# Kernel tuning notes

Hardware: AMD Instinct MI355X
Metric: run time of the kernel (lower is better)

The kernel has to match this reference:

```python
import jax, jax.numpy as jnp
import numpy as np

H = 384          # hidden_dim == filter_size == n_chans
N_BINS = 256
PRED_GRAD = 0.1
LN_EPS = 1e-5


def _conv1d_same(x_bct, w_oik, b):
    k = w_oik.shape[-1]
    p = (k - 1) // 2
    y = jax.lax.conv_general_dilated(
        x_bct, w_oik, window_strides=(1,), padding=[(p, p)],
        dimension_numbers=("NCT", "OIT", "NCT"))
    return y + b[None, :, None]


def _ln_last(x, g, b):  # LayerNorm over last dim
    m = jnp.mean(x, axis=-1, keepdims=True)
    v = jnp.var(x, axis=-1, keepdims=True)
    return (x - m) * jax.lax.rsqrt(v + LN_EPS) * g + b


def _ln_chan(x_bct, g, b):  # LayerNorm over channel dim (dim=1)
    m = jnp.mean(x_bct, axis=1, keepdims=True)
    v = jnp.var(x_bct, axis=1, keepdims=True)
    return (x_bct - m) * jax.lax.rsqrt(v + LN_EPS) * g[None, :, None] + b[None, :, None]


def _sin_pos(x0, dim):
    # fairseq SinusoidalPositionalEmbedding, padding_idx=0, applied to xs[...,0]
    mask = (x0 != 0).astype(jnp.int32)
    pos = jnp.cumsum(mask, axis=1) * mask                        # [B,T]
    half = dim // 2
    inv = jnp.exp(jnp.arange(half, dtype=jnp.float32) * (-(np.log(10000.0) / (half - 1))))
    ang = pos[..., None].astype(jnp.float32) * inv               # [B,T,half]
    pe = jnp.concatenate([jnp.sin(ang), jnp.cos(ang)], axis=-1)  # [B,T,dim]
    return jnp.where(pos[..., None] == 0, 0.0, pe)


def _duration_predictor(x, src_mask, w1, b1, g1, be1, w2, b2, g2, be2, lw, lb):
    h = _conv1d_same(jnp.swapaxes(x, 1, 2), w1, b1)
    h = _ln_last(jax.nn.relu(jnp.swapaxes(h, 1, 2)), g1, be1)
    h = _conv1d_same(jnp.swapaxes(h, 1, 2), w2, b2)
    h = _ln_last(jax.nn.relu(jnp.swapaxes(h, 1, 2)), g2, be2)
    out = (h @ lw + lb)[..., 0]                                  # [B,T]
    return jnp.where(src_mask, 0.0, out)


def _variance_predictor(x, cw, cb, g, b, lw, lb, alpha):
    pos = alpha * _sin_pos(x[..., 0], x.shape[-1])
    h = jnp.swapaxes(x + pos, 1, 2)                              # [B,C,T]
    for i in range(cw.shape[0]):
        h = _ln_chan(jax.nn.relu(_conv1d_same(h, cw[i], cb[i])), g[i], b[i])
    return jnp.swapaxes(h, 1, 2) @ lw + lb                       # [B,T,odim]


def _length_regulate(x, dur_int, max_len):
    B, T, _ = x.shape
    cum = jnp.cumsum(dur_int, axis=1)                            # [B,T]
    frames = jnp.arange(max_len)
    idx = jax.vmap(lambda c: jnp.searchsorted(c, frames, side="right"))(cum)
    idx = jnp.clip(idx, 0, T - 1)                                # [B,max_len]
    out = jnp.take_along_axis(x, idx[..., None], axis=1)         # [B,max_len,H]
    total = cum[:, -1]
    valid = frames[None, :] < total[:, None]
    out = jnp.where(valid[..., None], out, 0.0)
    mel_len = jnp.minimum(total, max_len)
    return out, mel_len


def setup_inputs() -> dict:
    key = jax.random.key(0)
    ks = iter(jax.random.split(key, 40))
    B, T = 32, 1024
    rnd = lambda s: 0.02 * jax.random.normal(next(ks), s, dtype=jnp.float32)
    inp = {
        "x": jax.random.normal(next(ks), (B, T, H), dtype=jnp.float32),
        "src_lens": jax.random.randint(next(ks), (B,), 0, T),
        "src_mask": jnp.zeros((B, T), dtype=bool),
        "max_len": 4096,
        # duration predictor (kernel=3)
        "dp_w1": rnd((H, H, 3)), "dp_b1": jnp.zeros((H,)),
        "dp_ln1_g": jnp.ones((H,)), "dp_ln1_b": jnp.zeros((H,)),
        "dp_w2": rnd((H, H, 3)), "dp_b2": jnp.zeros((H,)),
        "dp_ln2_g": jnp.ones((H,)), "dp_ln2_b": jnp.zeros((H,)),
        "dp_lw": rnd((H, 1)), "dp_lb": jnp.full((1,), 1.5),  # bias -> avg dur ~3.5
        # pitch predictor: 5 layers, kernel=5, odim=1 (use_uv=False)
        "pp_cw": rnd((5, H, H, 5)), "pp_cb": jnp.zeros((5, H)),
        "pp_g": jnp.ones((5, H)), "pp_b": jnp.zeros((5, H)),
        "pp_lw": rnd((H, 1)), "pp_lb": jnp.zeros((1,)), "pp_alpha": jnp.ones((1,)),
        # energy predictor: 2 layers, kernel=5, odim=1
        "ep_cw": rnd((2, H, H, 5)), "ep_cb": jnp.zeros((2, H)),
        "ep_g": jnp.ones((2, H)), "ep_b": jnp.zeros((2, H)),
        "ep_lw": rnd((H, 1)), "ep_lb": jnp.zeros((1,)), "ep_alpha": jnp.ones((1,)),
        # bins (requires_grad=False buffers) + embedding tables
        "pitch_bins": jnp.linspace(-4.0, 4.0, N_BINS - 1),
        "energy_bins": jnp.linspace(-4.0, 4.0, N_BINS - 1),
        "pitch_table": rnd((N_BINS, H)),
        "energy_table": rnd((N_BINS, H)),
    }
    return inp


def reference(x, src_lens, src_mask, max_len,
              dp_w1, dp_b1, dp_ln1_g, dp_ln1_b, dp_w2, dp_b2, dp_ln2_g, dp_ln2_b, dp_lw, dp_lb,
              pp_cw, pp_cb, pp_g, pp_b, pp_lw, pp_lb, pp_alpha,
              ep_cw, ep_cb, ep_g, ep_b, ep_lw, ep_lb, ep_alpha,
              pitch_bins, energy_bins, pitch_table, energy_table):
    # duration (inference path: no targets, controls = 1.0)
    log_d = _duration_predictor(x, src_mask, dp_w1, dp_b1, dp_ln1_g, dp_ln1_b,
                                dp_w2, dp_b2, dp_ln2_g, dp_ln2_b, dp_lw, dp_lb)
    dur = jnp.clip(jnp.round(jnp.exp(log_d) - 1.0), 0.0, None)
    dur_int = dur.astype(jnp.int32)

    # straight-through-style grad scaling on predictor inputs
    xg = jax.lax.stop_gradient(x) + PRED_GRAD * (x - jax.lax.stop_gradient(x))

    # phoneme-level pitch (use_uv=False -> squeeze, bucketize)
    pitch_pred = _variance_predictor(xg, pp_cw, pp_cb, pp_g, pp_b, pp_lw, pp_lb, pp_alpha)[..., 0]
    pitch_idx = jnp.searchsorted(pitch_bins, pitch_pred, side="left")  # torch.bucketize(right=False)
    pitch_emb = pitch_table[pitch_idx]

    # phoneme-level energy
    energy_pred = _variance_predictor(xg, ep_cw, ep_cb, ep_g, ep_b, ep_lw, ep_lb, ep_alpha)[..., 0]
    energy_idx = jnp.searchsorted(energy_bins, energy_pred, side="left")
    energy_emb = energy_table[energy_idx]

    x_adapt = x + pitch_emb + energy_emb
    out, mel_len = _length_regulate(x_adapt, dur_int, int(max_len))
    return out, log_d, dur, pitch_pred, energy_pred, mel_len
```

## Files before the change

kernel.cpp:

```cpp
#include <hip/hip_runtime.h>
#include <cstdint>

#define HH 384
#define NBINS 256

typedef __attribute__((ext_vector_type(8))) short short8v;
typedef __attribute__((ext_vector_type(16))) float f32x16;
typedef __attribute__((ext_vector_type(4))) unsigned short ushort4v;

__device__ inline float4 ld4(const float* p){ return *(const float4*)p; }

__device__ inline unsigned short bf16_rne(float f){
  unsigned u = __float_as_uint(f);
  unsigned r = u + 0x7FFFu + ((u >> 16) & 1u);
  return (unsigned short)(r >> 16);
}
__device__ inline float bf16_to_f(unsigned short h){
  return __uint_as_float(((unsigned)h) << 16);
}

__global__ __launch_bounds__(1024) void pos_kernel(const float* __restrict__ x,
    int* __restrict__ pos, int T)
{
  __shared__ int s[1024];
  int b = blockIdx.x, tid = threadIdx.x;
  int m = 0;
  if (tid < T) m = (x[((size_t)b*T + tid)*HH] != 0.f) ? 1 : 0;
  s[tid] = m;
  __syncthreads();
  for (int off = 1; off < 1024; off <<= 1){
    int add = (tid >= off) ? s[tid-off] : 0;
    __syncthreads();
    s[tid] += add;
    __syncthreads();
  }
  if (tid < T) pos[(size_t)b*T + tid] = s[tid] * m;
}

__global__ __launch_bounds__(HH) void add_pe_kernel(const float* __restrict__ x,
    const int* __restrict__ pos, const float* __restrict__ alpha,
    float* __restrict__ out)
{
  int row = blockIdx.x; int i = threadIdx.x;
  int p = pos[row];
  float pe = 0.f;
  if (p != 0){
    int j = (i < HH/2) ? i : i - HH/2;
    float inv = expf((float)j * -0.04822167734018944f);
    float ang = (float)p * inv;
    pe = (i < HH/2) ? sinf(ang) : cosf(ang);
  }
  out[(size_t)row*HH + i] = x[(size_t)row*HH + i] + alpha[0]*pe;
}

template<int K>
__global__ __launch_bounds__(256) void wtrans_kernel(const float* __restrict__ w,
    unsigned short* __restrict__ whi, unsigned short* __restrict__ wlo)
{
  int gid = blockIdx.x*256 + threadIdx.x;
  if (gid >= 384*384) return;
  int o = gid / 384, i = gid - (gid/384)*384;
  int c = i >> 4, half = (i >> 3) & 1, jj = i & 7;
  #pragma unroll
  for (int k = 0; k < K; ++k){
    float v = w[((size_t)o*384 + i)*K + k];
    unsigned short hi = bf16_rne(v);
    unsigned short lo = bf16_rne(v - bf16_to_f(hi));
    int s = k*24 + c;
    size_t dst = ((size_t)(s*2 + half)*384 + o)*8 + jj;
    whi[dst] = hi; wlo[dst] = lo;
  }
}

template<int K>
__global__ __launch_bounds__(256) void conv_mfma_kernel(
    const float* __restrict__ in, const unsigned short* __restrict__ whi,
    const unsigned short* __restrict__ wlo, const float* __restrict__ bias,
    const float* __restrict__ g, const float* __restrict__ be,
    float* __restrict__ out, int T)
{
  constexpr int M  = 32;
  constexpr int P  = (K-1)/2;
  constexpr int RT = M + K - 1;
  constexpr int NS = 24*K;
  constexpr int LDP = 392;
  __shared__ unsigned short xs_hi[(RT+1)*LDP];
  __shared__ unsigned short xs_lo[(RT+1)*LDP];
  __shared__ float ps[4][M], pq[4][M];

  int ntile = T / M;
  int b  = blockIdx.x / ntile;
  int t0 = (blockIdx.x % ntile) * M;
  int tid = threadIdx.x;
  const float* inb = in + (size_t)b*T*HH;

  {
    constexpr int TOT4 = RT*384/4;
    for (int e4 = tid; e4 < TOT4; e4 += 256){
      int r = e4 / 96, c4 = (e4 - r*96)*4;
      int t = t0 + r - P;
      float4 v = (t >= 0 && t < T) ? ld4(&inb[(size_t)t*HH + c4])
                                   : make_float4(0.f,0.f,0.f,0.f);
      float va[4] = {v.x, v.y, v.z, v.w};
      ushort4v h, l;
      #pragma unroll
      for (int q = 0; q < 4; ++q){
        unsigned short hq = bf16_rne(va[q]);
        h[q] = hq;
        l[q] = bf16_rne(va[q] - bf16_to_f(hq));
      }
      *(ushort4v*)&xs_hi[r*LDP + c4] = h;
      *(ushort4v*)&xs_lo[r*LDP + c4] = l;
    }
  }
  __syncthreads();

  int wv = tid >> 6, ln = tid & 63;
  int l31 = ln & 31, hl = ln >> 5;
  int o0 = wv * 96;

  const unsigned short* bhp = whi + ((size_t)hl*384 + o0 + l31)*8;
  const unsigned short* blp = wlo + ((size_t)hl*384 + o0 + l31)*8;
  int ab = l31*LDP + hl*8;

  f32x16 acc[3];
  #pragma unroll
  for (int nt = 0; nt < 3; ++nt){
    float bv = bias[o0 + nt*32 + l31];
    #pragma unroll
    for (int r = 0; r < 16; ++r) acc[nt][r] = bv;
  }

  short8v B0h[3], B0l[3], B1h[3], B1l[3];
  short8v A0h, A0l, A1h, A1l;

  #pragma unroll
  for (int nt = 0; nt < 3; ++nt){
    B0h[nt] = *(const short8v*)(bhp + nt*256);
    B0l[nt] = *(const short8v*)(blp + nt*256);
  }
  A0h = *(const short8v*)&xs_hi[ab];
  A0l = *(const short8v*)&xs_lo[ab];

  int aoffN = ab, ccN = 0;

#define CONV_STEP(CAh, CAl, CBh, CBl, NAh, NAl, NBh, NBl)                     \
  do {                                                                        \
    bhp += 6144; blp += 6144;                                                 \
    aoffN += 16; if (++ccN == 24){ ccN = 0; aoffN += LDP - 384; }             \
    _Pragma("unroll")                                                         \
    for (int nt = 0; nt < 3; ++nt){                                           \
      (NBh)[nt] = *(const short8v*)(bhp + nt*256);                            \
      (NBl)[nt] = *(const short8v*)(blp + nt*256);                            \
    }                                                                         \
    (NAh) = *(const short8v*)&xs_hi[aoffN];                                   \
    (NAl) = *(const short8v*)&xs_lo[aoffN];                                   \
    __builtin_amdgcn_sched_barrier(0);                                        \
    __builtin_amdgcn_s_setprio(1);                                            \
    _Pragma("unroll")                                                         \
    for (int nt = 0; nt < 3; ++nt)                                            \
      acc[nt] = __builtin_amdgcn_mfma_f32_32x32x16_bf16((CAh), (CBh)[nt], acc[nt], 0,0,0); \
    _Pragma("unroll")                                                         \
    for (int nt = 0; nt < 3; ++nt)                                            \
      acc[nt] = __builtin_amdgcn_mfma_f32_32x32x16_bf16((CAh), (CBl)[nt], acc[nt], 0,0,0); \
    _Pragma("unroll")                                                         \
    for (int nt = 0; nt < 3; ++nt)                                            \
      acc[nt] = __builtin_amdgcn_mfma_f32_32x32x16_bf16((CAl), (CBh)[nt], acc[nt], 0,0,0); \
    __builtin_amdgcn_s_setprio(0);                                            \
  } while(0)

  for (int s = 0; s < NS; s += 2){
    CONV_STEP(A0h, A0l, B0h, B0l, A1h, A1l, B1h, B1l);
    CONV_STEP(A1h, A1l, B1h, B1l, A0h, A0l, B0h, B0l);
  }
#undef CONV_STEP

  float gv[3], bev[3];
  #pragma unroll
  for (int nt = 0; nt < 3; ++nt){
    gv[nt]  = g[o0 + nt*32 + l31];
    bev[nt] = be[o0 + nt*32 + l31];
  }

  #pragma unroll
  for (int r = 0; r < 16; ++r){
    float s1 = 0.f, s2 = 0.f;
    #pragma unroll
    for (int nt = 0; nt < 3; ++nt){
      float v = fmaxf(acc[nt][r], 0.f);
      acc[nt][r] = v;
      s1 += v; s2 += v*v;
    }
    s1 += __shfl_xor(s1, 1);  s2 += __shfl_xor(s2, 1);
    s1 += __shfl_xor(s1, 2);  s2 += __shfl_xor(s2, 2);
    s1 += __shfl_xor(s1, 4);  s2 += __shfl_xor(s2, 4);
    s1 += __shfl_xor(s1, 8);  s2 += __shfl_xor(s2, 8);
    s1 += __shfl_xor(s1, 16); s2 += __shfl_xor(s2, 16);
    if (l31 == 0){
      int t = (r&3) + 8*(r>>2) + 4*hl;
      ps[wv][t] = s1; pq[wv][t] = s2;
    }
  }
  __syncthreads();

  #pragma unroll
  for (int r = 0; r < 16; ++r){
    int t = (r&3) + 8*(r>>2) + 4*hl;
    float s1 = ps[0][t] + ps[1][t] + ps[2][t] + ps[3][t];
    float s2 = pq[0][t] + pq[1][t] + pq[2][t] + pq[3][t];
    float mn  = s1 * (1.f/HH);
    float var = fmaxf(s2 * (1.f/HH) - mn*mn, 0.f);
    float rr  = rsqrtf(var + 1e-5f);
    float* orow = out + ((size_t)b*T + t0 + t)*HH;
    #pragma unroll
    for (int nt = 0; nt < 3; ++nt)
      orow[o0 + nt*32 + l31] = (acc[nt][r] - mn)*rr*gv[nt] + bev[nt];
  }
}

__global__ __launch_bounds__(256) void proj_var_kernel(const float* __restrict__ h,
    const float* __restrict__ lw, const float* __restrict__ lb,
    const float* __restrict__ bins, float* __restrict__ pred,
    int* __restrict__ idx, int nrows)
{
  int lane = threadIdx.x & 63, wid = threadIdx.x >> 6;
  int wave = blockIdx.x*4 + wid, nw = gridDim.x*4;
  float lwr[6];
  #pragma unroll
  for (int j = 0; j < 6; ++j) lwr[j] = lw[lane + 64*j];
  float lbv = lb[0];
  for (int row = wave; row < nrows; row += nw){
    const float* hr = h + (size_t)row*HH;
    float s = 0.f;
    #pragma unroll
    for (int j = 0; j < 6; ++j) s = fmaf(hr[lane + 64*j], lwr[j], s);
    #pragma unroll
    for (int off = 32; off; off >>= 1) s += __shfl_xor(s, off);
    if (lane == 0){
      float v = s + lbv;
      pred[row] = v;
      int lo = 0, hi = NBINS - 1;
      while (lo < hi){ int mid = (lo + hi) >> 1; if (bins[mid] < v) lo = mid + 1; else hi = mid; }
      idx[row] = lo;
    }
  }
}

__global__ __launch_bounds__(256) void proj_dur_kernel(const float* __restrict__ h,
    const float* __restrict__ lw, const float* __restrict__ lb,
    const unsigned char* __restrict__ mask, float* __restrict__ logd,
    float* __restrict__ durf, int* __restrict__ duri, int nrows)
{
  int lane = threadIdx.x & 63, wid = threadIdx.x >> 6;
  int wave = blockIdx.x*4 + wid, nw = gridDim.x*4;
  float lwr[6];
  #pragma unroll
  for (int j = 0; j < 6; ++j) lwr[j] = lw[lane + 64*j];
  float lbv = lb[0];
  for (int row = wave; row < nrows; row += nw){
    const float* hr = h + (size_t)row*HH;
    float s = 0.f;
    #pragma unroll
    for (int j = 0; j < 6; ++j) s = fmaf(hr[lane + 64*j], lwr[j], s);
    #pragma unroll
    for (int off = 32; off; off >>= 1) s += __shfl_xor(s, off);
    if (lane == 0){
      float v = s + lbv;
      if (mask[row]) v = 0.f;
      logd[row] = v;
      float d = fmaxf(rintf(expf(v) - 1.f), 0.f);
      durf[row] = d;
      duri[row] = (int)d;
    }
  }
}

__global__ __launch_bounds__(1024) void cumsum_kernel(const int* __restrict__ duri,
    int* __restrict__ cum, float* __restrict__ mel, int T, int ML)
{
  __shared__ int s[1024];
  int b = blockIdx.x, tid = threadIdx.x;
  s[tid] = (tid < T) ? duri[(size_t)b*T + tid] : 0;
  __syncthreads();
  for (int off = 1; off < 1024; off <<= 1){
    int add = (tid >= off) ? s[tid-off] : 0;
    __syncthreads();
    s[tid] += add;
    __syncthreads();
  }
  if (tid < T) cum[(size_t)b*T + tid] = s[tid];
  if (tid == T-1) mel[b] = (float)min(s[tid], ML);
}

__global__ __launch_bounds__(256) void xadapt_kernel(const float* __restrict__ x,
    const int* __restrict__ ip, const int* __restrict__ ie,
    const float* __restrict__ pt, const float* __restrict__ et,
    float* __restrict__ xa, int nrows)
{
  int gid = blockIdx.x*256 + threadIdx.x;
  int n4 = nrows * (HH/4);
  if (gid >= n4) return;
  int row = gid / (HH/4);
  int c = gid - row*(HH/4);
  float4 xv = ((const float4*)x)[gid];
  const float4* pr = (const float4*)(pt + (size_t)ip[row]*HH);
  const float4* er = (const float4*)(et + (size_t)ie[row]*HH);
  float4 pv = pr[c], ev = er[c];
  ((float4*)xa)[gid] = make_float4(xv.x+pv.x+ev.x, xv.y+pv.y+ev.y,
                                   xv.z+pv.z+ev.z, xv.w+pv.w+ev.w);
}

__global__ __launch_bounds__(256) void lr_kernel(const float* __restrict__ xa,
    const int* __restrict__ cum, float* __restrict__ out, int T, int ML)
{
  constexpr int FR = 32;
  __shared__ int scum[1024];
  __shared__ int sidx[FR];
  __shared__ int svalid[FR];
  int b  = blockIdx.y;
  int f0 = blockIdx.x * FR;
  for (int i = threadIdx.x; i < T; i += 256) scum[i] = cum[(size_t)b*T + i];
  __syncthreads();
  int total = scum[T-1];
  if (threadIdx.x < FR){
    int f = f0 + threadIdx.x;
    int lo = 0, hi = T;
    while (lo < hi){ int mid = (lo + hi) >> 1; if (scum[mid] <= f) lo = mid + 1; else hi = mid; }
    sidx[threadIdx.x] = min(lo, T-1);
    svalid[threadIdx.x] = (f < total) ? 1 : 0;
  }
  __syncthreads();
  #pragma unroll
  for (int it = 0; it < FR*(HH/4)/256; ++it){
    int item = it*256 + threadIdx.x;
    int fl = item / (HH/4);
    int c  = item - fl*(HH/4);
    int f  = f0 + fl;
    if (f >= ML) continue;
    float4 v = make_float4(0.f,0.f,0.f,0.f);
    if (svalid[fl]) v = ((const float4*)(xa + ((size_t)b*T + sidx[fl])*HH))[c];
    ((float4*)(out + ((size_t)b*ML + f)*HH))[c] = v;
  }
}

extern "C" void kernel_launch(void* const* d_in, const int* in_sizes, int n_in,
                              void* d_out, int out_size, void* d_ws, size_t ws_size,
                              hipStream_t stream)
{
  const float* x        = (const float*)d_in[0];
  const unsigned char* src_mask = (const unsigned char*)d_in[2];
  const float* dp_w1 = (const float*)d_in[4];
  const float* dp_b1 = (const float*)d_in[5];
  const float* dp_g1 = (const float*)d_in[6];
  const float* dp_be1= (const float*)d_in[7];
  const float* dp_w2 = (const float*)d_in[8];
  const float* dp_b2 = (const float*)d_in[9];
  const float* dp_g2 = (const float*)d_in[10];
  const float* dp_be2= (const float*)d_in[11];
  const float* dp_lw = (const float*)d_in[12];
  const float* dp_lb = (const float*)d_in[13];
  const float* pp_cw = (const float*)d_in[14];
  const float* pp_cb = (const float*)d_in[15];
  const float* pp_g  = (const float*)d_in[16];
  const float* pp_b  = (const float*)d_in[17];
  const float* pp_lw = (const float*)d_in[18];
  const float* pp_lb = (const float*)d_in[19];
  const float* pp_alpha = (const float*)d_in[20];
  const float* ep_cw = (const float*)d_in[21];
  const float* ep_cb = (const float*)d_in[22];
  const float* ep_g  = (const float*)d_in[23];
  const float* ep_b  = (const float*)d_in[24];
  const float* ep_lw = (const float*)d_in[25];
  const float* ep_lb = (const float*)d_in[26];
  const float* ep_alpha = (const float*)d_in[27];
  const float* pbins = (const float*)d_in[28];
  const float* ebins = (const float*)d_in[29];
  const float* ptab  = (const float*)d_in[30];
  const float* etab  = (const float*)d_in[31];

  int B = in_sizes[1];
  int T = in_sizes[0] / (B*HH);
  int ML = (int)(((long long)out_size - B - 4LL*B*T) / ((long long)B*HH));
  size_t rows = (size_t)B*T;

  float* bufA = (float*)d_ws;
  float* bufB = bufA + rows*HH;
  int* pos    = (int*)(bufB + rows*HH);
  int* idx_p  = pos + rows;
  int* idx_e  = idx_p + rows;
  int* dur_i  = idx_e + rows;
  int* cum    = dur_i + rows;

  float* out0    = (float*)d_out;
  float* logd    = out0 + (size_t)B*ML*HH;
  float* durf    = logd + rows;
  float* pitchp  = durf + rows;
  float* energyp = pitchp + rows;
  float* mel     = energyp + rows;

  unsigned short* wsc = (unsigned short*)d_out;
  const size_t K5S = (size_t)120*6144;
  const size_t K3S = (size_t)72*6144;
  size_t woff = 0;
  unsigned short *pph[5], *ppl[5], *eph[2], *epl[2], *dph[2], *dpl[2];
  for (int l = 0; l < 5; ++l){ pph[l] = wsc + woff; woff += K5S; ppl[l] = wsc + woff; woff += K5S; }
  for (int l = 0; l < 2; ++l){ eph[l] = wsc + woff; woff += K5S; epl[l] = wsc + woff; woff += K5S; }
  for (int l = 0; l < 2; ++l){ dph[l] = wsc + woff; woff += K3S; dpl[l] = wsc + woff; woff += K3S; }

  int wt_grid = (384*384 + 255)/256;
  for (int l = 0; l < 5; ++l)
    wtrans_kernel<5><<<wt_grid, 256, 0, stream>>>(pp_cw + (size_t)l*HH*HH*5, pph[l], ppl[l]);
  for (int l = 0; l < 2; ++l)
    wtrans_kernel<5><<<wt_grid, 256, 0, stream>>>(ep_cw + (size_t)l*HH*HH*5, eph[l], epl[l]);
  wtrans_kernel<3><<<wt_grid, 256, 0, stream>>>(dp_w1, dph[0], dpl[0]);
  wtrans_kernel<3><<<wt_grid, 256, 0, stream>>>(dp_w2, dph[1], dpl[1]);

  int conv_grid = B * (T / 32);

  pos_kernel<<<B, 1024, 0, stream>>>(x, pos, T);

  add_pe_kernel<<<(int)rows, HH, 0, stream>>>(x, pos, pp_alpha, bufA);
  {
    float* src = bufA; float* dst = bufB;
    for (int l = 0; l < 5; ++l){
      conv_mfma_kernel<5><<<conv_grid, 256, 0, stream>>>(src, pph[l], ppl[l],
          pp_cb + (size_t)l*HH, pp_g + (size_t)l*HH, pp_b + (size_t)l*HH, dst, T);
      float* t2 = dst; dst = src; src = t2;
    }
    proj_var_kernel<<<256, 256, 0, stream>>>(src, pp_lw, pp_lb, pbins,
                                             pitchp, idx_p, (int)rows);
  }

  add_pe_kernel<<<(int)rows, HH, 0, stream>>>(x, pos, ep_alpha, bufA);
  {
    float* src = bufA; float* dst = bufB;
    for (int l = 0; l < 2; ++l){
      conv_mfma_kernel<5><<<conv_grid, 256, 0, stream>>>(src, eph[l], epl[l],
          ep_cb + (size_t)l*HH, ep_g + (size_t)l*HH, ep_b + (size_t)l*HH, dst, T);
      float* t2 = dst; dst = src; src = t2;
    }
    proj_var_kernel<<<256, 256, 0, stream>>>(src, ep_lw, ep_lb, ebins,
                                             energyp, idx_e, (int)rows);
  }

  conv_mfma_kernel<3><<<conv_grid, 256, 0, stream>>>(x, dph[0], dpl[0],
      dp_b1, dp_g1, dp_be1, bufB, T);
  conv_mfma_kernel<3><<<conv_grid, 256, 0, stream>>>(bufB, dph[1], dpl[1],
      dp_b2, dp_g2, dp_be2, bufA, T);
  proj_dur_kernel<<<256, 256, 0, stream>>>(bufA, dp_lw, dp_lb, src_mask,
                                           logd, durf, dur_i, (int)rows);

  cumsum_kernel<<<B, 1024, 0, stream>>>(dur_i, cum, mel, T, ML);

  xadapt_kernel<<<(int)((rows*(HH/4) + 255)/256), 256, 0, stream>>>(
      x, idx_p, idx_e, ptab, etab, bufB, (int)rows);

  lr_kernel<<<dim3(ML/32, B), 256, 0, stream>>>(bufB, cum, out0, T, ML);
}
```

Baseline: 1.579 ms.

## Double conv time tile to 64 rows with 512 threads and deeper prefetch

The conv kernel now processes 64 time rows per block using 8 waves: two row groups share each weight column slice, so every weight fragment loaded from global memory serves twice as many outputs. The software pipeline now prefetches two steps ahead with triple-buffered registers. Weight transform launches are merged into one launch per predictor, and each layer's weight buffer is padded by two extra slices so the deeper prefetch can read past the end safely. The costs are higher register pressure, fewer blocks for small T, and a requirement that T be a multiple of 64.

```diff
diff --git a/kernel.cpp b/kernel.cpp
--- a/kernel.cpp
+++ b/kernel.cpp
@@ -55,48 +55,55 @@
 
 template<int K>
 __global__ __launch_bounds__(256) void wtrans_kernel(const float* __restrict__ w,
-    unsigned short* __restrict__ whi, unsigned short* __restrict__ wlo)
-{
+    unsigned short* __restrict__ dst, int nlayers)
+{
+  constexpr int SPL = (24*K + 2) * 6144;
+  const int per = 384*384;
   int gid = blockIdx.x*256 + threadIdx.x;
-  if (gid >= 384*384) return;
-  int o = gid / 384, i = gid - (gid/384)*384;
+  if (gid >= nlayers*per) return;
+  int l = gid / per, rem = gid - l*per;
+  int o = rem / 384, i = rem - (rem/384)*384;
+  unsigned short* whi = dst + (size_t)l*2*SPL;
+  unsigned short* wlo = whi + SPL;
+  const float* wl = w + (size_t)l*384*384*K;
   int c = i >> 4, half = (i >> 3) & 1, jj = i & 7;
   #pragma unroll
   for (int k = 0; k < K; ++k){
-    float v = w[((size_t)o*384 + i)*K + k];
+    float v = wl[((size_t)o*384 + i)*K + k];
     unsigned short hi = bf16_rne(v);
     unsigned short lo = bf16_rne(v - bf16_to_f(hi));
     int s = k*24 + c;
-    size_t dst = ((size_t)(s*2 + half)*384 + o)*8 + jj;
-    whi[dst] = hi; wlo[dst] = lo;
+    size_t d = ((size_t)(s*2 + half)*384 + o)*8 + jj;
+    whi[d] = hi; wlo[d] = lo;
   }
 }
 
 template<int K>
-__global__ __launch_bounds__(256) void conv_mfma_kernel(
+__global__ __launch_bounds__(512) void conv_mfma_kernel(
     const float* __restrict__ in, const unsigned short* __restrict__ whi,
     const unsigned short* __restrict__ wlo, const float* __restrict__ bias,
     const float* __restrict__ g, const float* __restrict__ be,
     float* __restrict__ out, int T)
 {
-  constexpr int M  = 32;
+  constexpr int MT = 64;
   constexpr int P  = (K-1)/2;
-  constexpr int RT = M + K - 1;
+  constexpr int RT = MT + K - 1;
+  constexpr int RA = RT + 2;
   constexpr int NS = 24*K;
   constexpr int LDP = 392;
-  __shared__ unsigned short xs_hi[(RT+1)*LDP];
-  __shared__ unsigned short xs_lo[(RT+1)*LDP];
-  __shared__ float ps[4][M], pq[4][M];
-
-  int ntile = T / M;
+  __shared__ unsigned short xs_hi[RA*LDP];
+  __shared__ unsigned short xs_lo[RA*LDP];
+  __shared__ float ps[8][32], pq[8][32];
+
+  int ntile = T / MT;
   int b  = blockIdx.x / ntile;
-  int t0 = (blockIdx.x % ntile) * M;
+  int t0 = (blockIdx.x % ntile) * MT;
   int tid = threadIdx.x;
   const float* inb = in + (size_t)b*T*HH;
 
   {
-    constexpr int TOT4 = RT*384/4;
-    for (int e4 = tid; e4 < TOT4; e4 += 256){
+    constexpr int TOT4 = RT*96;
+    for (int e4 = tid; e4 < TOT4; e4 += 512){
       int r = e4 / 96, c4 = (e4 - r*96)*4;
       int t = t0 + r - P;
       float4 v = (t >= 0 && t < T) ? ld4(&inb[(size_t)t*HH + c4])
@@ -117,11 +124,13 @@
 
   int wv = tid >> 6, ln = tid & 63;
   int l31 = ln & 31, hl = ln >> 5;
-  int o0 = wv * 96;
+  int nw = wv & 3, rg = wv >> 2;
+  int o0 = nw * 96;
 
   const unsigned short* bhp = whi + ((size_t)hl*384 + o0 + l31)*8;
   const unsigned short* blp = wlo + ((size_t)hl*384 + o0 + l31)*8;
-  int ab = l31*LDP + hl*8;
+  int aoff = (rg*32 + l31)*LDP + hl*8;
+  int cc = 0;
 
   f32x16 acc[3];
   #pragma unroll
@@ -131,49 +140,59 @@
     for (int r = 0; r < 16; ++r) acc[nt][r] = bv;
   }
 
-  short8v B0h[3], B0l[3], B1h[3], B1l[3];
-  short8v A0h, A0l, A1h, A1l;
+  short8v B0h[3], B0l[3], B1h[3], B1l[3], B2h[3], B2l[3];
+  short8v A0h, A0l, A1h, A1l, A2h, A2l;
+
+#define ADV do{ bhp += 6144; blp += 6144; aoff += 16;                        \
+                if (++cc == 24){ cc = 0; aoff += LDP - 384; } }while(0)
 
   #pragma unroll
   for (int nt = 0; nt < 3; ++nt){
     B0h[nt] = *(const short8v*)(bhp + nt*256);
     B0l[nt] = *(const short8v*)(blp + nt*256);
   }
-  A0h = *(const short8v*)&xs_hi[ab];
-  A0l = *(const short8v*)&xs_lo[ab];
-
-  int aoffN = ab, ccN = 0;
-
-#define CONV_STEP(CAh, CAl, CBh, CBl, NAh, NAl, NBh, NBl)                     \
-  do {                                                                        \
-    bhp += 6144; blp += 6144;                                                 \
-    aoffN += 16; if (++ccN == 24){ ccN = 0; aoffN += LDP - 384; }             \
-    _Pragma("unroll")                                                         \
-    for (int nt = 0; nt < 3; ++nt){                                           \
-      (NBh)[nt] = *(const short8v*)(bhp + nt*256);                            \
-      (NBl)[nt] = *(const short8v*)(blp + nt*256);                            \
-    }                                                                         \
-    (NAh) = *(const short8v*)&xs_hi[aoffN];                                   \
-    (NAl) = *(const short8v*)&xs_lo[aoffN];                                   \
-    __builtin_amdgcn_sched_barrier(0);                                        \
-    __builtin_amdgcn_s_setprio(1);                                            \
-    _Pragma("unroll")                                                         \
-    for (int nt = 0; nt < 3; ++nt)                                            \
-      acc[nt] = __builtin_amdgcn_mfma_f32_32x32x16_bf16((CAh), (CBh)[nt], acc[nt], 0,0,0); \
-    _Pragma("unroll")                                                         \
-    for (int nt = 0; nt < 3; ++nt)                                            \
-      acc[nt] = __builtin_amdgcn_mfma_f32_32x32x16_bf16((CAh), (CBl)[nt], acc[nt], 0,0,0); \
-    _Pragma("unroll")                                                         \
-    for (int nt = 0; nt < 3; ++nt)                                            \
-      acc[nt] = __builtin_amdgcn_mfma_f32_32x32x16_bf16((CAl), (CBh)[nt], acc[nt], 0,0,0); \
-    __builtin_amdgcn_s_setprio(0);                                            \
+  A0h = *(const short8v*)&xs_hi[aoff];
+  A0l = *(const short8v*)&xs_lo[aoff];
+  ADV;
+  #pragma unroll
+  for (int nt = 0; nt < 3; ++nt){
+    B1h[nt] = *(const short8v*)(bhp + nt*256);
+    B1l[nt] = *(const short8v*)(blp + nt*256);
+  }
+  A1h = *(const short8v*)&xs_hi[aoff];
+  A1l = *(const short8v*)&xs_lo[aoff];
+  ADV;
+
+#define PHASE(NBh,NBl,NAh,NAl,CBh,CBl,CAh,CAl) do{                           \
+    _Pragma("unroll")                                                        \
+    for (int nt = 0; nt < 3; ++nt){                                          \
+      NBh[nt] = *(const short8v*)(bhp + nt*256);                             \
+      NBl[nt] = *(const short8v*)(blp + nt*256);                             \
+    }                                                                        \
+    NAh = *(const short8v*)&xs_hi[aoff];                                     \
+    NAl = *(const short8v*)&xs_lo[aoff];                                     \
+    ADV;                                                                     \
+    __builtin_amdgcn_sched_barrier(0);                                       \
+    __builtin_amdgcn_s_setprio(1);                                           \
+    _Pragma("unroll")                                                        \
+    for (int nt = 0; nt < 3; ++nt)                                           \
+      acc[nt] = __builtin_amdgcn_mfma_f32_32x32x16_bf16(CAh, CBh[nt], acc[nt], 0,0,0); \
+    _Pragma("unroll")                                                        \
+    for (int nt = 0; nt < 3; ++nt)                                           \
+      acc[nt] = __builtin_amdgcn_mfma_f32_32x32x16_bf16(CAh, CBl[nt], acc[nt], 0,0,0); \
+    _Pragma("unroll")                                                        \
+    for (int nt = 0; nt < 3; ++nt)                                           \
+      acc[nt] = __builtin_amdgcn_mfma_f32_32x32x16_bf16(CAl, CBh[nt], acc[nt], 0,0,0); \
+    __builtin_amdgcn_s_setprio(0);                                           \
   } while(0)
 
-  for (int s = 0; s < NS; s += 2){
-    CONV_STEP(A0h, A0l, B0h, B0l, A1h, A1l, B1h, B1l);
-    CONV_STEP(A1h, A1l, B1h, B1l, A0h, A0l, B0h, B0l);
-  }
-#undef CONV_STEP
+  for (int s = 0; s < NS; s += 3){
+    PHASE(B2h,B2l,A2h,A2l, B0h,B0l,A0h,A0l);
+    PHASE(B0h,B0l,A0h,A0l, B1h,B1l,A1h,A1l);
+    PHASE(B1h,B1l,A1h,A1l, B2h,B2l,A2h,A2l);
+  }
+#undef PHASE
+#undef ADV
 
   float gv[3], bev[3];
   #pragma unroll
@@ -206,12 +225,12 @@
   #pragma unroll
   for (int r = 0; r < 16; ++r){
     int t = (r&3) + 8*(r>>2) + 4*hl;
-    float s1 = ps[0][t] + ps[1][t] + ps[2][t] + ps[3][t];
-    float s2 = pq[0][t] + pq[1][t] + pq[2][t] + pq[3][t];
+    float s1 = ps[rg*4+0][t] + ps[rg*4+1][t] + ps[rg*4+2][t] + ps[rg*4+3][t];
+    float s2 = pq[rg*4+0][t] + pq[rg*4+1][t] + pq[rg*4+2][t] + pq[rg*4+3][t];
     float mn  = s1 * (1.f/HH);
     float var = fmaxf(s2 * (1.f/HH) - mn*mn, 0.f);
     float rr  = rsqrtf(var + 1e-5f);
-    float* orow = out + ((size_t)b*T + t0 + t)*HH;
+    float* orow = out + ((size_t)b*T + t0 + rg*32 + t)*HH;
     #pragma unroll
     for (int nt = 0; nt < 3; ++nt)
       orow[o0 + nt*32 + l31] = (acc[nt][r] - mn)*rr*gv[nt] + bev[nt];
@@ -398,24 +417,21 @@
   float* energyp = pitchp + rows;
   float* mel     = energyp + rows;
 
-  unsigned short* wsc = (unsigned short*)d_out;
-  const size_t K5S = (size_t)120*6144;
-  const size_t K3S = (size_t)72*6144;
-  size_t woff = 0;
-  unsigned short *pph[5], *ppl[5], *eph[2], *epl[2], *dph[2], *dpl[2];
-  for (int l = 0; l < 5; ++l){ pph[l] = wsc + woff; woff += K5S; ppl[l] = wsc + woff; woff += K5S; }
-  for (int l = 0; l < 2; ++l){ eph[l] = wsc + woff; woff += K5S; epl[l] = wsc + woff; woff += K5S; }
-  for (int l = 0; l < 2; ++l){ dph[l] = wsc + woff; woff += K3S; dpl[l] = wsc + woff; woff += K3S; }
-
-  int wt_grid = (384*384 + 255)/256;
-  for (int l = 0; l < 5; ++l)
-    wtrans_kernel<5><<<wt_grid, 256, 0, stream>>>(pp_cw + (size_t)l*HH*HH*5, pph[l], ppl[l]);
-  for (int l = 0; l < 2; ++l)
-    wtrans_kernel<5><<<wt_grid, 256, 0, stream>>>(ep_cw + (size_t)l*HH*HH*5, eph[l], epl[l]);
-  wtrans_kernel<3><<<wt_grid, 256, 0, stream>>>(dp_w1, dph[0], dpl[0]);
-  wtrans_kernel<3><<<wt_grid, 256, 0, stream>>>(dp_w2, dph[1], dpl[1]);
-
-  int conv_grid = B * (T / 32);
+  const size_t SPL5 = (size_t)(24*5 + 2)*6144;
+  const size_t SPL3 = (size_t)(24*3 + 2)*6144;
+  unsigned short* wsc    = (unsigned short*)d_out;
+  unsigned short* pitchW = wsc;
+  unsigned short* enerW  = pitchW + 5*2*SPL5;
+  unsigned short* durW1  = enerW  + 2*2*SPL5;
+  unsigned short* durW2  = durW1  + 2*SPL3;
+
+  const int per = 384*384;
+  wtrans_kernel<5><<<(5*per + 255)/256, 256, 0, stream>>>(pp_cw, pitchW, 5);
+  wtrans_kernel<5><<<(2*per + 255)/256, 256, 0, stream>>>(ep_cw, enerW, 2);
+  wtrans_kernel<3><<<(per + 255)/256, 256, 0, stream>>>(dp_w1, durW1, 1);
+  wtrans_kernel<3><<<(per + 255)/256, 256, 0, stream>>>(dp_w2, durW2, 1);
+
+  int conv_grid = B * (T / 64);
 
   pos_kernel<<<B, 1024, 0, stream>>>(x, pos, T);
 
@@ -423,7 +439,8 @@
   {
     float* src = bufA; float* dst = bufB;
     for (int l = 0; l < 5; ++l){
-      conv_mfma_kernel<5><<<conv_grid, 256, 0, stream>>>(src, pph[l], ppl[l],
+      unsigned short* whi = pitchW + (size_t)l*2*SPL5;
+      conv_mfma_kernel<5><<<conv_grid, 512, 0, stream>>>(src, whi, whi + SPL5,
           pp_cb + (size_t)l*HH, pp_g + (size_t)l*HH, pp_b + (size_t)l*HH, dst, T);
       float* t2 = dst; dst = src; src = t2;
     }
@@ -435,7 +452,8 @@
   {
     float* src = bufA; float* dst = bufB;
     for (int l = 0; l < 2; ++l){
-      conv_mfma_kernel<5><<<conv_grid, 256, 0, stream>>>(src, eph[l], epl[l],
+      unsigned short* whi = enerW + (size_t)l*2*SPL5;
+      conv_mfma_kernel<5><<<conv_grid, 512, 0, stream>>>(src, whi, whi + SPL5,
           ep_cb + (size_t)l*HH, ep_g + (size_t)l*HH, ep_b + (size_t)l*HH, dst, T);
       float* t2 = dst; dst = src; src = t2;
     }
@@ -443,9 +461,9 @@
                                              energyp, idx_e, (int)rows);
   }
 
-  conv_mfma_kernel<3><<<conv_grid, 256, 0, stream>>>(x, dph[0], dpl[0],
+  conv_mfma_kernel<3><<<conv_grid, 512, 0, stream>>>(x, durW1, durW1 + SPL3,
       dp_b1, dp_g1, dp_be1, bufB, T);
-  conv_mfma_kernel<3><<<conv_grid, 256, 0, stream>>>(bufB, dph[1], dpl[1],
+  conv_mfma_kernel<3><<<conv_grid, 512, 0, stream>>>(bufB, durW2, durW2 + SPL3,
       dp_b2, dp_g2, dp_be2, bufA, T);
   proj_dur_kernel<<<256, 256, 0, stream>>>(bufA, dp_lw, dp_lb, src_mask,
                                            logd, durf, dur_i, (int)rows);
```

Result: slower. 1.654 ms (+4.7%).
